# Optimization experiments

Hardware: AMD Instinct MI355X
Metric: run time of the kernel (lower is better)

Reference implementation:

```python
import jax, jax.numpy as jnp
import numpy as np

EPS = 1e-5
NUM_PIXELS = 2  # M_Relax window half-width


def _conv(x, w, b, groups=1, pad=0):
    y = jax.lax.conv_general_dilated(
        x, w, (1, 1), [(pad, pad), (pad, pad)],
        dimension_numbers=("NCHW", "OIHW", "NCHW"),
        feature_group_count=groups)
    return y + b[None, :, None, None]


def _bn(x, g, bta, m, v):
    # eval-mode BatchNorm2d with running stats
    inv = jax.lax.rsqrt(v + EPS)
    return g[None, :, None, None] * (x - m[None, :, None, None]) * inv[None, :, None, None] + bta[None, :, None, None]


def _resb(x, w1, b1, w2, b2):
    y = _conv(x, w1, b1, groups=4, pad=1)
    y = jnp.where(y > 0, y, 0.1 * y)  # LeakyReLU(0.1)
    y = _conv(y, w2, b2, groups=4, pad=1)
    return y + x


def _relax(M):
    # M: (N, w, w); sum of shifts +-NUM_PIXELS along the row (dim 1)
    w = M.shape[1]
    P = jnp.pad(M, ((0, 0), (NUM_PIXELS, NUM_PIXELS), (0, 0)))
    out = P[:, 0:w, :]
    for k in range(1, 2 * NUM_PIXELS + 1):
        out = out + P[:, k:k + w, :]
    return out


def setup_inputs() -> dict:
    key = jax.random.key(0)
    ks = jax.random.split(key, 16)
    b, c, h, w = 4, 64, 128, 256
    c2 = 2 * c
    s = 0.05
    inp = {
        "x_left": jax.random.normal(ks[0], (b, c, h, w), jnp.float32),
        "x_right": jax.random.normal(ks[1], (b, c, h, w), jnp.float32),
        "conv1_w": jax.random.normal(ks[2], (c, c, 1, 1), jnp.float32) * s,
        "conv1_b": jnp.zeros((c,), jnp.float32),
        "conv2_w": jax.random.normal(ks[3], (c, c, 1, 1), jnp.float32) * s,
        "conv2_b": jnp.zeros((c,), jnp.float32),
        "bn_g": jnp.ones((c2,), jnp.float32),
        "bn_b": jnp.zeros((c2,), jnp.float32),
        "bn_m": jax.random.normal(ks[4], (c2,), jnp.float32) * 0.1,
        "bn_v": jax.random.uniform(ks[5], (c2,), jnp.float32) + 0.5,
        "rb_w1": jax.random.normal(ks[6], (c2, c2 // 4, 3, 3), jnp.float32) * s,
        "rb_b1": jnp.zeros((c2,), jnp.float32),
        "rb_w2": jax.random.normal(ks[7], (c2, c2 // 4, 3, 3), jnp.float32) * s,
        "rb_b2": jnp.zeros((c2,), jnp.float32),
        "bq_w": jax.random.normal(ks[8], (c, c, 1, 1), jnp.float32) * s,
        "bq_b": jnp.zeros((c,), jnp.float32),
        "bs_w": jax.random.normal(ks[9], (c, c, 1, 1), jnp.float32) * s,
        "bs_b": jnp.zeros((c,), jnp.float32),
    }
    return inp


def reference(x_left, x_right, conv1_w, conv1_b, conv2_w, conv2_b,
              bn_g, bn_b, bn_m, bn_v, rb_w1, rb_b1, rb_w2, rb_b2,
              bq_w, bq_b, bs_w, bs_b):
    b, c, h, w = x_left.shape
    cat_l = jnp.concatenate([_conv(x_left, conv1_w, conv1_b), x_left], axis=1)
    cat_r = jnp.concatenate([_conv(x_right, conv2_w, conv2_b), x_right], axis=1)
    Q = _conv(_resb(_bn(cat_l, bn_g, bn_b, bn_m, bn_v), rb_w1, rb_b1, rb_w2, rb_b2), bq_w, bq_b, groups=2)
    K = _conv(_resb(_bn(cat_r, bn_g, bn_b, bn_m, bn_v), rb_w1, rb_b1, rb_w2, rb_b2), bs_w, bs_b, groups=2)
    Q = Q - Q.mean(axis=3, keepdims=True)
    K = K - K.mean(axis=3, keepdims=True)
    # score: (b*h, w, w) -- per-epipolar-row cross-view attention
    Qr = Q.transpose(0, 2, 3, 1).reshape(b * h, w, c)
    Kr = K.transpose(0, 2, 1, 3).reshape(b * h, c, w)
    score = jnp.matmul(Qr, Kr)
    M_r2l = jax.nn.softmax(score, axis=-1)
    M_l2r = jax.nn.softmax(score.transpose(0, 2, 1), axis=-1)
    # validity maps via relaxed cycle-consistency (detached in original)
    V_l = jnp.einsum("nij,nji->ni", _relax(M_r2l), M_l2r)
    V_r = jnp.einsum("nij,nji->ni", _relax(M_l2r), M_r2l)
    V_l = jax.lax.stop_gradient(V_l).reshape(b, 1, h, w)
    V_r = jax.lax.stop_gradient(V_r).reshape(b, 1, h, w)
    V_l_t = jnp.tanh(5.0 * V_l)
    V_r_t = jnp.tanh(5.0 * V_r)
    xl = x_left.transpose(0, 2, 3, 1).reshape(b * h, w, c)
    xr = x_right.transpose(0, 2, 3, 1).reshape(b * h, w, c)
    x_lT = jnp.matmul(M_r2l, xr).reshape(b, h, w, c).transpose(0, 3, 1, 2)
    x_rT = jnp.matmul(M_l2r, xl).reshape(b, h, w, c).transpose(0, 3, 1, 2)
    out_left = x_left * (1.0 - V_l_t) + x_lT * V_l_t
    out_right = x_right * (1.0 - V_r_t) + x_rT * V_r_t
    return out_left, out_right
```

## Files before the change

kernel.cpp:

```cpp
#include <hip/hip_runtime.h>
#include <math.h>

#define BB 4
#define CC 64
#define C2 128
#define HH 128
#define WW 256
#define NN (BB*HH)
#define EPSBN 1e-5f

typedef _Float16 f16;
typedef _Float16 half8 __attribute__((ext_vector_type(8)));
typedef float f32x4 __attribute__((ext_vector_type(4)));

__global__ __launch_bounds__(256) void k_wprep(
    const float* __restrict__ w1, const float* __restrict__ w2,
    f16* __restrict__ wp1, f16* __restrict__ wp2)
{
    int g = blockIdx.x; int which = blockIdx.y;
    const float* src = which ? w2 : w1;
    f16* dst = which ? wp2 : wp1;
    for (int p = threadIdx.x; p < 9216; p += 256) {
        int mo = p / 288; int kr = p - mo*288;
        int ks = kr >> 5; int ic = kr & 31;
        dst[g*9216 + p] = (f16)src[((g*32 + mo)*32 + ic)*9 + ks];
    }
}

__global__ __launch_bounds__(256) void k_catbn_m(
    const float* __restrict__ x, const float* __restrict__ cw, const float* __restrict__ cb,
    const float* __restrict__ g, const float* __restrict__ bb_, const float* __restrict__ m,
    const float* __restrict__ v, f16* __restrict__ u)
{
    __shared__ f16 Xl[256][72];
    __shared__ f16 Wl[64][72];
    __shared__ float sS[64], sT[64], sS2[64], sT2[64];
    int n = blockIdx.x; int b = n >> 7; int h = n & 127; int t = threadIdx.x;
    for (int p = t; p < 2048; p += 256) {
        int idx = p * 2; int o = idx >> 6, i = idx & 63;
        union { f16 h[2]; unsigned int u1; } pr;
        pr.h[0] = (f16)cw[idx]; pr.h[1] = (f16)cw[idx + 1];
        *(unsigned int*)&Wl[o][i] = pr.u1;
    }
    if (t < 64) {
        float inv = rsqrtf(v[t] + EPSBN); float s = g[t] * inv;
        sS[t] = s; sT[t] = bb_[t] + s * (cb[t] - m[t]);
        float inv2 = rsqrtf(v[t + 64] + EPSBN); float s2 = g[t + 64] * inv2;
        sS2[t] = s2; sT2[t] = bb_[t + 64] - s2 * m[t + 64];
    }
    __syncthreads();
    f16* up = u + ((size_t)(n*256 + t)) * 128;
    for (int c8 = 0; c8 < 8; ++c8) {
        float xv8[8];
#pragma unroll
        for (int j = 0; j < 8; ++j)
            xv8[j] = x[(((b*64 + c8*8 + j)*128 + h) << 8) + t];
        union { f16 h[8]; uint4 v4; } pk;
#pragma unroll
        for (int j = 0; j < 8; ++j) {
            int c = c8*8 + j;
            pk.h[j] = (f16)(sS2[c]*xv8[j] + sT2[c]);
        }
        *(uint4*)(up + 64 + c8*8) = pk.v4;
#pragma unroll
        for (int j2 = 0; j2 < 4; ++j2) {
            union { f16 h[2]; unsigned int u1; } q;
            q.h[0] = (f16)xv8[j2*2]; q.h[1] = (f16)xv8[j2*2 + 1];
            *(unsigned int*)&Xl[t][c8*8 + j2*2] = q.u1;
        }
    }
    __syncthreads();
    int lane = t & 63, wv = t >> 6;
    int m16 = lane & 15, quad = lane >> 4;
    half8 af[4][2], bf[4][2];
#pragma unroll
    for (int mt = 0; mt < 4; ++mt)
#pragma unroll
        for (int kk = 0; kk < 2; ++kk)
            af[mt][kk] = *(const half8*)&Wl[mt*16 + m16][kk*32 + quad*8];
#pragma unroll
    for (int nt = 0; nt < 4; ++nt)
#pragma unroll
        for (int kk = 0; kk < 2; ++kk)
            bf[nt][kk] = *(const half8*)&Xl[wv*64 + nt*16 + m16][kk*32 + quad*8];
    f32x4 acc[4][4] = {};
#pragma unroll
    for (int mt = 0; mt < 4; ++mt)
#pragma unroll
        for (int nt = 0; nt < 4; ++nt) {
            acc[mt][nt] = __builtin_amdgcn_mfma_f32_16x16x32_f16(af[mt][0], bf[nt][0], acc[mt][nt], 0, 0, 0);
            acc[mt][nt] = __builtin_amdgcn_mfma_f32_16x16x32_f16(af[mt][1], bf[nt][1], acc[mt][nt], 0, 0, 0);
        }
#pragma unroll
    for (int mt = 0; mt < 4; ++mt) {
        int ocb = mt*16 + quad*4;
        float s4[4], t4[4];
        *(float4*)s4 = *(const float4*)&sS[ocb];
        *(float4*)t4 = *(const float4*)&sT[ocb];
#pragma unroll
        for (int nt = 0; nt < 4; ++nt) {
            int px = wv*64 + nt*16 + m16;
            union { f16 h[4]; uint2 u2; } ov;
#pragma unroll
            for (int r = 0; r < 4; ++r)
                ov.h[r] = (f16)(s4[r]*acc[mt][nt][r] + t4[r]);
            *(uint2*)(u + ((size_t)(n*256 + px))*128 + ocb) = ov.u2;
        }
    }
}

template<bool LEAKY, bool RES>
__global__ __launch_bounds__(256, 3) void k_conv3r(
    const f16* __restrict__ in, const f16* __restrict__ wp,
    const float* __restrict__ bias, const f16* __restrict__ res,
    f16* __restrict__ out)
{
    __shared__ f16 Xl[4*130*40];
    int b = blockIdx.x >> 6; int h0 = (blockIdx.x & 63) * 2;
    int g = blockIdx.y; int w0 = blockIdx.z * 128;
    int t = threadIdx.x;
    int lane = t & 63, wv = t >> 6;
    int m16 = lane & 15, quad = lane >> 4;
    const f16* wg = wp + g*9216;
    half8 af[2][9];
#pragma unroll
    for (int mt = 0; mt < 2; ++mt)
#pragma unroll
        for (int ks = 0; ks < 9; ++ks)
            af[mt][ks] = *(const half8*)(wg + (mt*16 + m16)*288 + ks*32 + quad*8);
    float bo[2][4];
#pragma unroll
    for (int mt = 0; mt < 2; ++mt)
#pragma unroll
        for (int r = 0; r < 4; ++r)
            bo[mt][r] = bias[g*32 + mt*16 + quad*4 + r];
    for (int idx = t; idx < 2080; idx += 256) {
        int r = idx / 520; int rem = idx - r*520; int p = rem >> 2; int q = rem & 3;
        int hr = h0 + r - 1; int wg2 = w0 + p - 1;
        uint4 val = make_uint4(0,0,0,0);
        if ((unsigned)wg2 < 256u && (unsigned)hr < 128u)
            val = *(const uint4*)(in + ((size_t)((b*128 + hr)*256 + wg2))*128 + g*32 + q*8);
        *(uint4*)&Xl[(r*130 + p)*40 + q*8] = val;
    }
    __syncthreads();
    int px0 = wv*32 + m16;
#pragma unroll
    for (int rr = 0; rr < 2; ++rr) {
        f32x4 acc[2][2] = {};
#pragma unroll
        for (int ks = 0; ks < 9; ++ks) {
            int ky = ks / 3, kx = ks - ky*3;
            half8 bf0 = *(const half8*)&Xl[((rr + ky)*130 + px0 + kx)*40 + quad*8];
            half8 bf1 = *(const half8*)&Xl[((rr + ky)*130 + px0 + 16 + kx)*40 + quad*8];
            acc[0][0] = __builtin_amdgcn_mfma_f32_16x16x32_f16(af[0][ks], bf0, acc[0][0], 0, 0, 0);
            acc[0][1] = __builtin_amdgcn_mfma_f32_16x16x32_f16(af[0][ks], bf1, acc[0][1], 0, 0, 0);
            acc[1][0] = __builtin_amdgcn_mfma_f32_16x16x32_f16(af[1][ks], bf0, acc[1][0], 0, 0, 0);
            acc[1][1] = __builtin_amdgcn_mfma_f32_16x16x32_f16(af[1][ks], bf1, acc[1][1], 0, 0, 0);
        }
        int h = h0 + rr;
#pragma unroll
        for (int mt = 0; mt < 2; ++mt)
#pragma unroll
            for (int nt = 0; nt < 2; ++nt) {
                int px = w0 + wv*32 + nt*16 + m16;
                int oc = g*32 + mt*16 + quad*4;
                size_t off = ((size_t)((b*128 + h)*256 + px))*128 + oc;
                float rv4[4] = {0.f, 0.f, 0.f, 0.f};
                if (RES) {
                    union { f16 h[4]; uint2 v2; } rrd;
                    rrd.v2 = *(const uint2*)(res + off);
#pragma unroll
                    for (int r = 0; r < 4; ++r) rv4[r] = (float)rrd.h[r];
                }
                union { f16 h[4]; uint2 v2; } ov;
#pragma unroll
                for (int r = 0; r < 4; ++r) {
                    float y = acc[mt][nt][r] + bo[mt][r];
                    if (LEAKY) y = y > 0.f ? y : 0.1f*y;
                    if (RES) y += rv4[r];
                    ov.h[r] = (f16)y;
                }
                *(uint2*)(out + off) = ov.v2;
            }
    }
}

__global__ __launch_bounds__(256, 2) void k_conv1x1m(
    const f16* __restrict__ in, const float* __restrict__ wgt,
    f16* __restrict__ outq)
{
    __shared__ f16 Xl[256][72];
    __shared__ f16 Wl[64][72];
    __shared__ float partial[4][64];
    __shared__ float meanS[64];
    int n = blockIdx.x; int t = threadIdx.x;
    int lane = t & 63, wv = t >> 6;
    int m16 = lane & 15, quad = lane >> 4;
    for (int p = t; p < 2048; p += 256) {
        int idx = p * 2; int o = idx >> 6, i = idx & 63;
        union { f16 h[2]; unsigned int u1; } pr;
        pr.h[0] = (f16)wgt[idx]; pr.h[1] = (f16)wgt[idx + 1];
        *(unsigned int*)&Wl[o][i] = pr.u1;
    }
    f32x4 acc[4][4] = {};
    const f16* rp = in + ((size_t)n*256 + t)*128;
    for (int g = 0; g < 2; ++g) {
#pragma unroll
        for (int i8 = 0; i8 < 8; ++i8)
            *(uint4*)&Xl[t][i8*8] = *(const uint4*)(rp + g*64 + i8*8);
        __syncthreads();
        half8 af[2][2], bf[4][2];
#pragma unroll
        for (int ml = 0; ml < 2; ++ml)
#pragma unroll
            for (int kk = 0; kk < 2; ++kk)
                af[ml][kk] = *(const half8*)&Wl[g*32 + ml*16 + m16][kk*32 + quad*8];
#pragma unroll
        for (int nt = 0; nt < 4; ++nt)
#pragma unroll
            for (int kk = 0; kk < 2; ++kk)
                bf[nt][kk] = *(const half8*)&Xl[wv*64 + nt*16 + m16][kk*32 + quad*8];
#pragma unroll
        for (int ml = 0; ml < 2; ++ml)
#pragma unroll
            for (int nt = 0; nt < 4; ++nt) {
                int mt = g*2 + ml;
                acc[mt][nt] = __builtin_amdgcn_mfma_f32_16x16x32_f16(af[ml][0], bf[nt][0], acc[mt][nt], 0, 0, 0);
                acc[mt][nt] = __builtin_amdgcn_mfma_f32_16x16x32_f16(af[ml][1], bf[nt][1], acc[mt][nt], 0, 0, 0);
            }
        __syncthreads();
    }
#pragma unroll
    for (int mt = 0; mt < 4; ++mt)
#pragma unroll
        for (int r = 0; r < 4; ++r) {
            float s = acc[mt][0][r] + acc[mt][1][r] + acc[mt][2][r] + acc[mt][3][r];
            s += __shfl_xor(s, 1); s += __shfl_xor(s, 2);
            s += __shfl_xor(s, 4); s += __shfl_xor(s, 8);
            if (m16 == 0) partial[wv][mt*16 + quad*4 + r] = s;
        }
    __syncthreads();
    if (t < 64)
        meanS[t] = (partial[0][t] + partial[1][t] + partial[2][t] + partial[3][t]) * (1.0f/256.0f);
    __syncthreads();
    f16* qp = outq + ((size_t)n*256)*64;
#pragma unroll
    for (int mt = 0; mt < 4; ++mt) {
        int ocb = mt*16 + quad*4;
        float m4[4]; *(float4*)m4 = *(const float4*)&meanS[ocb];
#pragma unroll
        for (int nt = 0; nt < 4; ++nt) {
            int px = wv*64 + nt*16 + m16;
            union { f16 h[4]; uint2 u2; } ov;
#pragma unroll
            for (int r = 0; r < 4; ++r)
                ov.h[r] = (f16)(acc[mt][nt][r] - m4[r]);
            *(uint2*)(qp + (size_t)px*64 + ocb) = ov.u2;
        }
    }
}

__device__ __forceinline__ void attn_pass3(
    const f16* __restrict__ Ap, const f16* __restrict__ Bp, char* pool,
    const float* __restrict__ myM, const float* __restrict__ myI,
    const float* __restrict__ oM,  const float* __restrict__ oI,
    const float* __restrict__ xB, const float* __restrict__ xP,
    float* __restrict__ outp, int b, int h, int t)
{
    f16 (*Pl)[40] = (f16(*)[40])pool;
    f16 (*Xl)[40] = (f16(*)[40])(pool + 20800);
    float* scr = (float*)(pool + 20800);
    float* Vv  = (float*)(pool + 22848);
    int lane = t & 63, wv = t >> 6;
    int m16 = lane & 15, quad = lane >> 4;
    int W = wv * 32;
    int r = t & 255, hc = t >> 8;
    int cbase = hc * 16;
    float rm = myM[r], ri = myI[r];
    int xc = t >> 3, xj = (t & 7) * 4;
    const float* xg = xB + ((size_t)(b*64 + xc)*128 + h)*256;
    half8 af[2][2];
#pragma unroll
    for (int mt = 0; mt < 2; ++mt)
#pragma unroll
        for (int kk = 0; kk < 2; ++kk)
            af[mt][kk] = *(const half8*)(Ap + (size_t)(W + mt*16 + m16)*64 + kk*32 + quad*8);
    f32x4 acc[2][4] = {};
    float vacc = 0.f;
    for (int kc = 0; kc < 256; kc += 32) {
        half8 bf[2][2];
#pragma unroll
        for (int nt = 0; nt < 2; ++nt)
#pragma unroll
            for (int kk = 0; kk < 2; ++kk)
                bf[nt][kk] = *(const half8*)(Bp + (size_t)(kc + nt*16 + m16)*64 + kk*32 + quad*8);
        f32x4 s1[2][2] = {};
#pragma unroll
        for (int mt = 0; mt < 2; ++mt)
#pragma unroll
            for (int nt = 0; nt < 2; ++nt) {
                s1[mt][nt] = __builtin_amdgcn_mfma_f32_16x16x32_f16(af[mt][0], bf[nt][0], s1[mt][nt], 0, 0, 0);
                s1[mt][nt] = __builtin_amdgcn_mfma_f32_16x16x32_f16(af[mt][1], bf[nt][1], s1[mt][nt], 0, 0, 0);
            }
        {
            float4 x4 = *(const float4*)(xg + kc + xj);
            union { f16 h[4]; uint2 v2; } px;
            px.h[0] = (f16)x4.x; px.h[1] = (f16)x4.y;
            px.h[2] = (f16)x4.z; px.h[3] = (f16)x4.w;
            *(uint2*)&Xl[xc][xj] = px.v2;
        }
#pragma unroll
        for (int mt = 0; mt < 2; ++mt)
#pragma unroll
            for (int nt = 0; nt < 2; ++nt)
#pragma unroll
                for (int rr = 0; rr < 4; ++rr)
                    Pl[W + mt*16 + quad*4 + rr + 2][nt*16 + m16] = (f16)s1[mt][nt][rr];
        __syncthreads();
        float sraw[16];
        char* pb = (char*)&Pl[r + 2][cbase];
        {
            half8 v0 = *(const half8*)pb;
            half8 v1 = *(const half8*)(pb + 16);
            half8 p0, p1;
#pragma unroll
            for (int e = 0; e < 8; ++e) {
                sraw[e] = (float)v0[e];
                p0[e] = (f16)(__expf(sraw[e] - rm) * ri);
            }
#pragma unroll
            for (int e = 0; e < 8; ++e) {
                sraw[8 + e] = (float)v1[e];
                p1[e] = (f16)(__expf(sraw[8 + e] - rm) * ri);
            }
            *(half8*)pb = p0; *(half8*)(pb + 16) = p1;
        }
        __syncthreads();
#pragma unroll
        for (int j8 = 0; j8 < 2; ++j8) {
            const char* wb = (const char*)&Pl[r][cbase + j8*8];
            half8 w0 = *(const half8*)(wb);
            half8 w1 = *(const half8*)(wb + 80);
            half8 w2 = *(const half8*)(wb + 160);
            half8 w3 = *(const half8*)(wb + 240);
            half8 w4 = *(const half8*)(wb + 320);
            half8 win = w0 + w1 + w2 + w3 + w4;
#pragma unroll
            for (int e = 0; e < 8; ++e) {
                int j = kc + cbase + j8*8 + e;
                float Bv = __expf(sraw[j8*8 + e] - oM[j]) * oI[j];
                vacc = fmaf((float)win[e], Bv, vacc);
            }
        }
        half8 pa[2], xb_[4];
#pragma unroll
        for (int mt = 0; mt < 2; ++mt)
            pa[mt] = *(const half8*)((const char*)&Pl[W + mt*16 + m16 + 2][0] + quad*16);
#pragma unroll
        for (int nt = 0; nt < 4; ++nt)
            xb_[nt] = *(const half8*)((const char*)&Xl[nt*16 + m16][0] + quad*16);
#pragma unroll
        for (int mt = 0; mt < 2; ++mt)
#pragma unroll
            for (int nt = 0; nt < 4; ++nt)
                acc[mt][nt] = __builtin_amdgcn_mfma_f32_16x16x32_f16(pa[mt], xb_[nt], acc[mt][nt], 0, 0, 0);
        __syncthreads();
    }
    scr[hc*256 + r] = vacc;
    __syncthreads();
    if (t < 256) Vv[t] = scr[t] + scr[256 + t];
    __syncthreads();
#pragma unroll
    for (int mt = 0; mt < 2; ++mt) {
        int i0 = W + mt*16 + quad*4;
        float v4[4];
        *(float4*)v4 = *(const float4*)&Vv[i0];
        float tv[4];
#pragma unroll
        for (int rr = 0; rr < 4; ++rr) tv[rr] = tanhf(5.f*v4[rr]);
#pragma unroll
        for (int nt = 0; nt < 4; ++nt) {
            int c = nt*16 + m16;
            size_t base = (((size_t)(b*64 + c)*128 + h) << 8) + i0;
            float xp4[4]; *(float4*)xp4 = *(const float4*)&xP[base];
            float o4[4];
#pragma unroll
            for (int rr = 0; rr < 4; ++rr)
                o4[rr] = xp4[rr]*(1.f - tv[rr]) + acc[mt][nt][rr]*tv[rr];
            *(float4*)&outp[base] = *(float4*)o4;
        }
    }
}

__global__ __launch_bounds__(512, 4) void k_attn3(
    const f16* __restrict__ Q, const f16* __restrict__ K,
    const float* __restrict__ xl, const float* __restrict__ xr,
    float* __restrict__ outL, float* __restrict__ outR)
{
    __shared__ __align__(16) char pool[25920];
    __shared__ float rmS[256], riS[256], cmS[256], ciS[256];
    float* colM = (float*)pool;
    float* colS = (float*)(pool + 8192);
    int n = blockIdx.x; int b = n >> 7; int h = n & 127;
    int t = threadIdx.x;
    int lane = t & 63, wv = t >> 6;
    int m16 = lane & 15, quad = lane >> 4;
    int W = wv * 32;

    const f16* ag = Q + (size_t)n*16384;
    const f16* bg = K + (size_t)n*16384;
    half8 af1[2][2];
#pragma unroll
    for (int mt = 0; mt < 2; ++mt)
#pragma unroll
        for (int kk = 0; kk < 2; ++kk)
            af1[mt][kk] = *(const half8*)(ag + (size_t)(W + mt*16 + m16)*64 + kk*32 + quad*8);
    float rowm[8], rows_[8];
#pragma unroll
    for (int i = 0; i < 8; ++i) { rowm[i] = -1e30f; rows_[i] = 0.f; }
    for (int jc = 0; jc < 256; jc += 64) {
        half8 bf1[4][2];
#pragma unroll
        for (int nt = 0; nt < 4; ++nt)
#pragma unroll
            for (int kk = 0; kk < 2; ++kk)
                bf1[nt][kk] = *(const half8*)(bg + (size_t)(jc + nt*16 + m16)*64 + kk*32 + quad*8);
        f32x4 acc1[2][4] = {};
#pragma unroll
        for (int mt = 0; mt < 2; ++mt)
#pragma unroll
            for (int nt = 0; nt < 4; ++nt) {
                acc1[mt][nt] = __builtin_amdgcn_mfma_f32_16x16x32_f16(af1[mt][0], bf1[nt][0], acc1[mt][nt], 0, 0, 0);
                acc1[mt][nt] = __builtin_amdgcn_mfma_f32_16x16x32_f16(af1[mt][1], bf1[nt][1], acc1[mt][nt], 0, 0, 0);
            }
#pragma unroll
        for (int mt = 0; mt < 2; ++mt)
#pragma unroll
            for (int nt = 0; nt < 4; ++nt)
#pragma unroll
                for (int r = 0; r < 4; ++r)
                    acc1[mt][nt][r] = (float)(f16)acc1[mt][nt][r];
#pragma unroll
        for (int mt = 0; mt < 2; ++mt)
#pragma unroll
            for (int r = 0; r < 4; ++r) {
                float lm = fmaxf(fmaxf(acc1[mt][0][r], acc1[mt][1][r]),
                                 fmaxf(acc1[mt][2][r], acc1[mt][3][r]));
                lm = fmaxf(lm, __shfl_xor(lm, 1));
                lm = fmaxf(lm, __shfl_xor(lm, 2));
                lm = fmaxf(lm, __shfl_xor(lm, 4));
                lm = fmaxf(lm, __shfl_xor(lm, 8));
                float le = __expf(acc1[mt][0][r] - lm) + __expf(acc1[mt][1][r] - lm)
                         + __expf(acc1[mt][2][r] - lm) + __expf(acc1[mt][3][r] - lm);
                le += __shfl_xor(le, 1); le += __shfl_xor(le, 2);
                le += __shfl_xor(le, 4); le += __shfl_xor(le, 8);
                int idx = mt*4 + r;
                float nm = fmaxf(rowm[idx], lm);
                rows_[idx] = rows_[idx]*__expf(rowm[idx] - nm) + le*__expf(lm - nm);
                rowm[idx] = nm;
            }
#pragma unroll
        for (int nt = 0; nt < 4; ++nt) {
            float lm = acc1[0][nt][0];
#pragma unroll
            for (int r = 1; r < 4; ++r) lm = fmaxf(lm, acc1[0][nt][r]);
#pragma unroll
            for (int r = 0; r < 4; ++r) lm = fmaxf(lm, acc1[1][nt][r]);
            lm = fmaxf(lm, __shfl_xor(lm, 16));
            lm = fmaxf(lm, __shfl_xor(lm, 32));
            float le = 0.f;
#pragma unroll
            for (int mt2 = 0; mt2 < 2; ++mt2)
#pragma unroll
                for (int r = 0; r < 4; ++r) le += __expf(acc1[mt2][nt][r] - lm);
            le += __shfl_xor(le, 16); le += __shfl_xor(le, 32);
            if (quad == 0) {
                int col = jc + nt*16 + m16;
                colM[wv*256 + col] = lm;
                colS[wv*256 + col] = le;
            }
        }
    }
    if (m16 == 0) {
#pragma unroll
        for (int mt = 0; mt < 2; ++mt)
#pragma unroll
            for (int r = 0; r < 4; ++r) {
                int row = W + mt*16 + quad*4 + r;
                rmS[row] = rowm[mt*4 + r];
                riS[row] = 1.0f / rows_[mt*4 + r];
            }
    }
    __syncthreads();
    if (t < 256) {
        float m = colM[t], s = colS[t];
#pragma unroll
        for (int w = 1; w < 8; ++w) {
            float m2 = colM[w*256 + t], s2 = colS[w*256 + t];
            float nm = fmaxf(m, m2);
            s = s*__expf(m - nm) + s2*__expf(m2 - nm);
            m = nm;
        }
        cmS[t] = m; ciS[t] = 1.0f / s;
    }
    __syncthreads();
    if (t < 10)       *(uint4*)(pool + t*16)              = make_uint4(0,0,0,0);
    else if (t < 20)  *(uint4*)(pool + 20640 + (t-10)*16) = make_uint4(0,0,0,0);

    attn_pass3(ag, bg, pool, rmS, riS, cmS, ciS, xr, xl, outL, b, h, t);
    __syncthreads();
    attn_pass3(bg, ag, pool, cmS, ciS, rmS, riS, xl, xr, outR, b, h, t);
}

extern "C" void kernel_launch(void* const* d_in, const int* in_sizes, int n_in,
                              void* d_out, int out_size, void* d_ws, size_t ws_size,
                              hipStream_t stream)
{
    const float* x_left  = (const float*)d_in[0];
    const float* x_right = (const float*)d_in[1];
    const float* conv1_w = (const float*)d_in[2];
    const float* conv1_b = (const float*)d_in[3];
    const float* conv2_w = (const float*)d_in[4];
    const float* conv2_b = (const float*)d_in[5];
    const float* bn_g    = (const float*)d_in[6];
    const float* bn_b    = (const float*)d_in[7];
    const float* bn_m    = (const float*)d_in[8];
    const float* bn_v    = (const float*)d_in[9];
    const float* rb_w1   = (const float*)d_in[10];
    const float* rb_b1   = (const float*)d_in[11];
    const float* rb_w2   = (const float*)d_in[12];
    const float* rb_b2   = (const float*)d_in[13];
    const float* bq_w    = (const float*)d_in[14];
    const float* bs_w    = (const float*)d_in[16];

    f16* W16 = (f16*)d_ws;
    f16* u  = W16;
    f16* y1 = W16 + 16777216;
    f16* r  = W16 + 33554432;
    f16* Qh = W16 + 67108864;
    f16* Kh = W16 + 75497472;
    f16* Wp1 = W16 + 84934656;
    f16* Wp2 = W16 + 84971520;

    float* out_left  = (float*)d_out;
    float* out_right = (float*)d_out + 8388608;

    k_wprep<<<dim3(4, 2), 256, 0, stream>>>(rb_w1, rb_w2, Wp1, Wp2);

    k_catbn_m<<<NN, 256, 0, stream>>>(x_left, conv1_w, conv1_b, bn_g, bn_b, bn_m, bn_v, u);
    k_conv3r<true,  false><<<dim3(256, 4, 2), 256, 0, stream>>>(u, Wp1, rb_b1, nullptr, y1);
    k_conv3r<false, true ><<<dim3(256, 4, 2), 256, 0, stream>>>(y1, Wp2, rb_b2, u, r);
    k_conv1x1m<<<NN, 256, 0, stream>>>(r, bq_w, Qh);

    k_catbn_m<<<NN, 256, 0, stream>>>(x_right, conv2_w, conv2_b, bn_g, bn_b, bn_m, bn_v, u);
    k_conv3r<true,  false><<<dim3(256, 4, 2), 256, 0, stream>>>(u, Wp1, rb_b1, nullptr, y1);
    k_conv3r<false, true ><<<dim3(256, 4, 2), 256, 0, stream>>>(y1, Wp2, rb_b2, u, r);
    k_conv1x1m<<<NN, 256, 0, stream>>>(r, bs_w, Kh);

    k_attn3<<<NN, 512, 0, stream>>>(Qh, Kh, x_left, x_right, out_left, out_right);
}
```

Baseline: 471.2 us.

## Fuse softmax exp into score store and defer row-max shuffle reduction

In the attention pass, each lane now computes the softmax probability right as it writes the MFMA score tile to LDS. Raw scores go to a separate LDS buffer, which removes one __syncthreads and a read-modify-write pass per 32-column chunk. In the first pass, the per-chunk cross-lane row max/sum shuffle reduction is replaced by per-lane online accumulation, merged once at the end with a 16-lane shuffle tree. The trade-off is LDS use per block growing from about 26KB to about 46KB, which may reduce occupancy under the 4-block launch bound.

```diff
diff --git a/kernel.cpp b/kernel.cpp
--- a/kernel.cpp
+++ b/kernel.cpp
@@ -260,7 +260,7 @@
     }
 }
 
-__device__ __forceinline__ void attn_pass3(
+__device__ __forceinline__ void attn_pass5(
     const f16* __restrict__ Ap, const f16* __restrict__ Bp, char* pool,
     const float* __restrict__ myM, const float* __restrict__ myI,
     const float* __restrict__ oM,  const float* __restrict__ oI,
@@ -268,15 +268,15 @@
     float* __restrict__ outp, int b, int h, int t)
 {
     f16 (*Pl)[40] = (f16(*)[40])pool;
-    f16 (*Xl)[40] = (f16(*)[40])(pool + 20800);
-    float* scr = (float*)(pool + 20800);
-    float* Vv  = (float*)(pool + 22848);
+    f16 (*Sr)[40] = (f16(*)[40])(pool + 20800);
+    f16 (*Xl)[40] = (f16(*)[40])(pool + 41280);
+    float* scr = (float*)(pool + 41280);
+    float* Vv  = (float*)(pool + 43328);
     int lane = t & 63, wv = t >> 6;
     int m16 = lane & 15, quad = lane >> 4;
     int W = wv * 32;
     int r = t & 255, hc = t >> 8;
     int cbase = hc * 16;
-    float rm = myM[r], ri = myI[r];
     int xc = t >> 3, xj = (t & 7) * 4;
     const float* xg = xB + ((size_t)(b*64 + xc)*128 + h)*256;
     half8 af[2][2];
@@ -285,6 +285,15 @@
 #pragma unroll
         for (int kk = 0; kk < 2; ++kk)
             af[mt][kk] = *(const half8*)(Ap + (size_t)(W + mt*16 + m16)*64 + kk*32 + quad*8);
+    float rmv[8], riv[8];
+#pragma unroll
+    for (int mt = 0; mt < 2; ++mt)
+#pragma unroll
+        for (int rr = 0; rr < 4; ++rr) {
+            int row = W + mt*16 + quad*4 + rr;
+            rmv[mt*4 + rr] = myM[row];
+            riv[mt*4 + rr] = myI[row];
+        }
     f32x4 acc[2][4] = {};
     float vacc = 0.f;
     for (int kc = 0; kc < 256; kc += 32) {
@@ -314,27 +323,14 @@
 #pragma unroll
             for (int nt = 0; nt < 2; ++nt)
 #pragma unroll
-                for (int rr = 0; rr < 4; ++rr)
-                    Pl[W + mt*16 + quad*4 + rr + 2][nt*16 + m16] = (f16)s1[mt][nt][rr];
-        __syncthreads();
-        float sraw[16];
-        char* pb = (char*)&Pl[r + 2][cbase];
-        {
-            half8 v0 = *(const half8*)pb;
-            half8 v1 = *(const half8*)(pb + 16);
-            half8 p0, p1;
-#pragma unroll
-            for (int e = 0; e < 8; ++e) {
-                sraw[e] = (float)v0[e];
-                p0[e] = (f16)(__expf(sraw[e] - rm) * ri);
-            }
-#pragma unroll
-            for (int e = 0; e < 8; ++e) {
-                sraw[8 + e] = (float)v1[e];
-                p1[e] = (f16)(__expf(sraw[8 + e] - rm) * ri);
-            }
-            *(half8*)pb = p0; *(half8*)(pb + 16) = p1;
-        }
+                for (int rr = 0; rr < 4; ++rr) {
+                    int row = W + mt*16 + quad*4 + rr;
+                    int col = nt*16 + m16;
+                    f16 hv = (f16)s1[mt][nt][rr];
+                    Sr[row][col] = hv;
+                    int ridx = mt*4 + rr;
+                    Pl[row + 2][col] = (f16)(__expf((float)hv - rmv[ridx]) * riv[ridx]);
+                }
         __syncthreads();
 #pragma unroll
         for (int j8 = 0; j8 < 2; ++j8) {
@@ -345,10 +341,11 @@
             half8 w3 = *(const half8*)(wb + 240);
             half8 w4 = *(const half8*)(wb + 320);
             half8 win = w0 + w1 + w2 + w3 + w4;
+            half8 rw = *(const half8*)&Sr[r][cbase + j8*8];
 #pragma unroll
             for (int e = 0; e < 8; ++e) {
                 int j = kc + cbase + j8*8 + e;
-                float Bv = __expf(sraw[j8*8 + e] - oM[j]) * oI[j];
+                float Bv = __expf((float)rw[e] - oM[j]) * oI[j];
                 vacc = fmaf((float)win[e], Bv, vacc);
             }
         }
@@ -392,12 +389,12 @@
     }
 }
 
-__global__ __launch_bounds__(512, 4) void k_attn3(
+__global__ __launch_bounds__(512, 4) void k_attn5(
     const f16* __restrict__ Q, const f16* __restrict__ K,
     const float* __restrict__ xl, const float* __restrict__ xr,
     float* __restrict__ outL, float* __restrict__ outR)
 {
-    __shared__ __align__(16) char pool[25920];
+    __shared__ __align__(16) char pool[46400];
     __shared__ float rmS[256], riS[256], cmS[256], ciS[256];
     float* colM = (float*)pool;
     float* colS = (float*)(pool + 8192);
@@ -444,19 +441,14 @@
         for (int mt = 0; mt < 2; ++mt)
 #pragma unroll
             for (int r = 0; r < 4; ++r) {
-                float lm = fmaxf(fmaxf(acc1[mt][0][r], acc1[mt][1][r]),
-                                 fmaxf(acc1[mt][2][r], acc1[mt][3][r]));
-                lm = fmaxf(lm, __shfl_xor(lm, 1));
-                lm = fmaxf(lm, __shfl_xor(lm, 2));
-                lm = fmaxf(lm, __shfl_xor(lm, 4));
-                lm = fmaxf(lm, __shfl_xor(lm, 8));
-                float le = __expf(acc1[mt][0][r] - lm) + __expf(acc1[mt][1][r] - lm)
-                         + __expf(acc1[mt][2][r] - lm) + __expf(acc1[mt][3][r] - lm);
-                le += __shfl_xor(le, 1); le += __shfl_xor(le, 2);
-                le += __shfl_xor(le, 4); le += __shfl_xor(le, 8);
                 int idx = mt*4 + r;
+                float v0 = acc1[mt][0][r], v1 = acc1[mt][1][r];
+                float v2 = acc1[mt][2][r], v3 = acc1[mt][3][r];
+                float lm = fmaxf(fmaxf(v0, v1), fmaxf(v2, v3));
                 float nm = fmaxf(rowm[idx], lm);
-                rows_[idx] = rows_[idx]*__expf(rowm[idx] - nm) + le*__expf(lm - nm);
+                rows_[idx] = rows_[idx]*__expf(rowm[idx] - nm)
+                           + __expf(v0 - nm) + __expf(v1 - nm)
+                           + __expf(v2 - nm) + __expf(v3 - nm);
                 rowm[idx] = nm;
             }
 #pragma unroll
@@ -481,6 +473,19 @@
             }
         }
     }
+#pragma unroll
+    for (int idx = 0; idx < 8; ++idx) {
+        float m = rowm[idx], s = rows_[idx];
+#pragma unroll
+        for (int off = 1; off < 16; off <<= 1) {
+            float m2 = __shfl_xor(m, off);
+            float s2 = __shfl_xor(s, off);
+            float nm = fmaxf(m, m2);
+            s = s*__expf(m - nm) + s2*__expf(m2 - nm);
+            m = nm;
+        }
+        rowm[idx] = m; rows_[idx] = s;
+    }
     if (m16 == 0) {
 #pragma unroll
         for (int mt = 0; mt < 2; ++mt)
@@ -507,9 +512,9 @@
     if (t < 10)       *(uint4*)(pool + t*16)              = make_uint4(0,0,0,0);
     else if (t < 20)  *(uint4*)(pool + 20640 + (t-10)*16) = make_uint4(0,0,0,0);
 
-    attn_pass3(ag, bg, pool, rmS, riS, cmS, ciS, xr, xl, outL, b, h, t);
-    __syncthreads();
-    attn_pass3(bg, ag, pool, cmS, ciS, rmS, riS, xl, xr, outR, b, h, t);
+    attn_pass5(ag, bg, pool, rmS, riS, cmS, ciS, xr, xl, outL, b, h, t);
+    __syncthreads();
+    attn_pass5(bg, ag, pool, cmS, ciS, rmS, riS, xl, xr, outR, b, h, t);
 }
 
 extern "C" void kernel_launch(void* const* d_in, const int* in_sizes, int n_in,
@@ -557,5 +562,5 @@
     k_conv3r<false, true ><<<dim3(256, 4, 2), 256, 0, stream>>>(y1, Wp2, rb_b2, u, r);
     k_conv1x1m<<<NN, 256, 0, stream>>>(r, bs_w, Kh);
 
-    k_attn3<<<NN, 512, 0, stream>>>(Qh, Kh, x_left, x_right, out_left, out_right);
-}
+    k_attn5<<<NN, 512, 0, stream>>>(Qh, Kh, x_left, x_right, out_left, out_right);
+}
```

Result: no change. 470.6 us (-0.1%).
